# Kernel optimization log

Measured on AMD Instinct MI355X. Metric: run time of the kernel, lower is better.

## Reference

```python
import jax, jax.numpy as jnp
import numpy as np

NUM_HEADS = 4

def setup_inputs() -> dict:
    key = jax.random.key(0)
    ks = jax.random.split(key, 9)
    C = 256
    def w(k, shape, scale):
        return jax.random.normal(k, shape, dtype=jnp.float32) * scale
    s = 1.0 / np.sqrt(C)
    return {
        'x':  w(ks[0], (1, C, 48, 48), 1.0),
        'Wq': w(ks[1], (C, C), s), 'bq': w(ks[2], (C,), 0.01),
        'Wk': w(ks[3], (C, C), s), 'bk': w(ks[4], (C,), 0.01),
        'Wv': w(ks[5], (C, C), s), 'bv': w(ks[6], (C,), 0.01),
        'Wo': w(ks[7], (C, C), s), 'bo': w(ks[8], (C,), 0.01),
    }

def reference(x, Wq, bq, Wk, bk, Wv, bv, Wo, bo):
    # x: [B, C, H, W] (NCHW like torch). 1x1 convs == per-pixel matmuls in NHWC.
    B, C, H, W = x.shape
    nh = NUM_HEADS
    xt = jnp.transpose(x, (0, 2, 3, 1))                 # [B,H,W,C]
    q = xt @ Wq.T + bq                                  # [B,H,W,Ck]
    k = xt @ Wk.T + bk                                  # [B,H,W,Ck]
    v = xt @ Wv.T + bv                                  # [B,H,W,Cv]
    dk = q.shape[-1] // nh
    dv = v.shape[-1] // nh
    # split heads then FULLY flatten (batch*H*W*heads), as in the original
    qf = q.reshape(B * H * W * nh, dk) / jnp.sqrt(jnp.float32(dk))
    kf = k.reshape(B * H * W * nh, dk)
    vf = v.reshape(B * H * W * nh, dv)
    A = jax.nn.softmax(qf @ kf.T, axis=1)               # [N,N], N = B*H*W*nh
    # dropout is identity in eval mode
    O = A @ vf                                          # [N,dv]
    O = O.reshape(B, H, W, nh * dv)                     # heads folded back into channels
    out = O @ Wo.T + bo                                 # 1x1 output conv
    return jnp.transpose(out, (0, 3, 1, 2))             # [B,Cout,H,W]
```

## Files before the change

kernel.cpp:

```cpp
#include <hip/hip_runtime.h>
#include <stdint.h>

typedef __attribute__((ext_vector_type(4))) float f32x4;
typedef __attribute__((ext_vector_type(8))) short bf16x8;

#define MFMA(a, b, c) __builtin_amdgcn_mfma_f32_16x16x32_bf16(a, b, c, 0, 0, 0)

__device__ __forceinline__ short f2b(float f) {
    uint32_t u = __builtin_bit_cast(uint32_t, f);
    u += 0x7fffu + ((u >> 16) & 1u);
    return (short)(u >> 16);
}

__device__ __forceinline__ float ex2(float x) {
    float r; asm("v_exp_f32 %0, %1" : "=v"(r) : "v"(x)); return r;
}
__device__ __forceinline__ uint32_t cvtpk(float lo, float hi) {
    uint32_t r; asm("v_cvt_pk_bf16_f32 %0, %1, %2" : "=v"(r) : "v"(lo), "v"(hi)); return r;
}

typedef __attribute__((address_space(1))) const uint32_t gu32;
typedef __attribute__((address_space(3))) uint32_t su32;
__device__ __forceinline__ void stage16(const void* g, void* s) {
    __builtin_amdgcn_global_load_lds((gu32*)g, (su32*)s, 16, 0, 0);
}

__device__ __forceinline__ int FSW(int r) { return (r & 3) | (((r >> 3) & 1) << 2); }

#define QSCALE 0.1803368801111601f

__global__ __launch_bounds__(256) void k_prep(
    const float* __restrict__ x,
    const float* __restrict__ Wq, const float* __restrict__ Wk,
    const float* __restrict__ Wv, const float* __restrict__ Wo,
    short* __restrict__ Wall, short* __restrict__ xt) {
    __shared__ float tile[64][65];
    if (blockIdx.x < 1024) {
        int idx = blockIdx.x * 256 + threadIdx.x;
        int row = idx >> 8, col = idx & 255;
        float v;
        if (row < 256)      v = Wq[row * 256 + col];
        else if (row < 512) v = Wk[(row - 256) * 256 + col];
        else if (row < 768) v = Wv[(row - 512) * 256 + col];
        else                v = Wo[(row - 768) * 256 + col];
        Wall[idx] = f2b(v);
    } else {
        int b = blockIdx.x - 1024;
        int pbase = (b % 36) * 64, cbase = (b / 36) * 64;
        int tx = threadIdx.x & 63, tq = threadIdx.x >> 6;
        #pragma unroll
        for (int r = 0; r < 16; r++) {
            int row = tq * 16 + r;
            tile[row][tx] = x[(cbase + row) * 2304 + pbase + tx];
        }
        __syncthreads();
        #pragma unroll
        for (int r = 0; r < 16; r++) {
            int prow = tq * 16 + r;
            xt[(pbase + prow) * 256 + cbase + tx] = f2b(tile[tx][prow]);
        }
    }
}

__global__ __launch_bounds__(256) void k_gemm_qkv(
    const short* __restrict__ Wall, const short* __restrict__ xt,
    const float* __restrict__ bq, const float* __restrict__ bk, const float* __restrict__ bv,
    short* __restrict__ Qf, short* __restrict__ Kf, short* __restrict__ Vt) {
    int t = threadIdx.x, wave = t >> 6, lane = t & 63, lr = lane & 15, lg = lane >> 4;
    int obase = blockIdx.x * 64 + wave * 16;
    int pbase = blockIdx.y * 64;
    const short* arow  = Wall + (obase + lr) * 256 + lg * 8;
    const short* brow0 = xt + (pbase +  0 + lr) * 256 + lg * 8;
    const short* brow1 = xt + (pbase + 16 + lr) * 256 + lg * 8;
    const short* brow2 = xt + (pbase + 32 + lr) * 256 + lg * 8;
    const short* brow3 = xt + (pbase + 48 + lr) * 256 + lg * 8;
    f32x4 acc0 = {0,0,0,0}, acc1 = {0,0,0,0}, acc2 = {0,0,0,0}, acc3 = {0,0,0,0};
    #pragma unroll
    for (int ks = 0; ks < 8; ks++) {
        bf16x8 a = *(const bf16x8*)(arow + ks * 32);
        acc0 = MFMA(a, *(const bf16x8*)(brow0 + ks * 32), acc0);
        acc1 = MFMA(a, *(const bf16x8*)(brow1 + ks * 32), acc1);
        acc2 = MFMA(a, *(const bf16x8*)(brow2 + ks * 32), acc2);
        acc3 = MFMA(a, *(const bf16x8*)(brow3 + ks * 32), acc3);
    }
    int w_idx = obase >> 8;
    const float* bias = (w_idx == 0) ? bq : (w_idx == 1) ? bk : bv;
    f32x4 accs[4] = {acc0, acc1, acc2, acc3};
    #pragma unroll
    for (int i = 0; i < 4; i++) {
        int o = obase + 4 * lg + i;
        int oo = o & 255;
        float b = bias[oo];
        int h = oo >> 6, d = oo & 63;
        #pragma unroll
        for (int ct = 0; ct < 4; ct++) {
            int p = pbase + ct * 16 + lr;
            float val = accs[ct][i] + b;
            int n = p * 4 + h;
            if (w_idx == 0)      Qf[n * 64 + d] = f2b(val * QSCALE);
            else if (w_idx == 1) Kf[n * 64 + d] = f2b(val);
            else                 Vt[d * 9216 + n] = f2b(val);
        }
    }
}

__global__ __launch_bounds__(256) void k_attn(
    const short* __restrict__ Qf, const short* __restrict__ Kf,
    const short* __restrict__ Vt, int keysPer, int ntiles,
    float* __restrict__ pm, float* __restrict__ ps, float* __restrict__ pacc) {
    __shared__ short ktile[2][4096];
    __shared__ short vtile[2][4096];
    int t = threadIdx.x, wave = t >> 6, lane = t & 63, lr = lane & 15, lg = lane >> 4;
    int kb = blockIdx.y;
    int qbase = blockIdx.x * 64 + wave * 16;
    int kstart = kb * keysPer;

    const short* qrow = Qf + (qbase + lr) * 64 + lg * 8;
    bf16x8 q0 = *(const bf16x8*)(qrow);
    bf16x8 q1 = *(const bf16x8*)(qrow + 32);

    bf16x8 ones;
    #pragma unroll
    for (int i = 0; i < 8; i++) ones[i] = (short)0x3F80;

    int sr = lane >> 3, slot = lane & 7;
    int srow0 = wave * 16 + sr, srow1 = srow0 + 8;
    int col0 = (slot ^ FSW(srow0)) << 4;
    int col1 = (slot ^ FSW(srow1)) << 4;
    const char* kS0 = (const char*)Kf + (size_t)(kstart + srow0) * 128 + col0;
    const char* kS1 = (const char*)Kf + (size_t)(kstart + srow1) * 128 + col1;
    const char* vS0 = (const char*)Vt + (size_t)srow0 * 18432 + (size_t)kstart * 2 + col0;
    const char* vS1 = (const char*)Vt + (size_t)srow1 * 18432 + (size_t)kstart * 2 + col1;
    short* kD0[2] = { &ktile[0][wave * 1024], &ktile[1][wave * 1024] };
    short* kD1[2] = { kD0[0] + 512, kD0[1] + 512 };
    short* vD0[2] = { &vtile[0][wave * 1024], &vtile[1][wave * 1024] };
    short* vD1[2] = { vD0[0] + 512, vD0[1] + 512 };

    int perm = (lr & 3) + 8 * (lr >> 2);
    int cb = lg * 16;
    int kOffA0 = perm * 128       + (cb        ^ (FSW(perm) << 4));
    int kOffA1 = perm * 128       + ((cb + 64) ^ (FSW(perm) << 4));
    int kOffB0 = (perm + 4) * 128 + (cb        ^ (FSW(perm + 4) << 4));
    int kOffB1 = (perm + 4) * 128 + ((cb + 64) ^ (FSW(perm + 4) << 4));
    int vOff   = lr * 128         + (cb        ^ (FSW(lr) << 4));

    float mA = 0.f;
    f32x4 zv = {0,0,0,0};
    f32x4 cin = zv;
    f32x4 acc0 = zv, acc1 = zv, acc2 = zv, acc3 = zv, sacc = zv;

    stage16(kS0, kD0[0]); stage16(kS1, kD1[0]);
    stage16(vS0, vD0[0]); stage16(vS1, vD1[0]);

    for (int tt = 0; tt < ntiles; tt++) {
        __syncthreads();
        int buf = tt & 1;
        if (tt + 1 < ntiles) {
            size_t ko = (size_t)(tt + 1) * 8192, vo = (size_t)(tt + 1) * 128;
            stage16(kS0 + ko, kD0[buf ^ 1]); stage16(kS1 + ko, kD1[buf ^ 1]);
            stage16(vS0 + vo, vD0[buf ^ 1]); stage16(vS1 + vo, vD1[buf ^ 1]);
        }
        const char* kt = (const char*)&ktile[buf][0];
        const char* vt = (const char*)&vtile[buf][0];

        bf16x8 kA0 = *(const bf16x8*)(kt + kOffA0);
        bf16x8 kA1 = *(const bf16x8*)(kt + kOffA1);
        bf16x8 kB0 = *(const bf16x8*)(kt + kOffB0);
        bf16x8 kB1 = *(const bf16x8*)(kt + kOffB1);
        f32x4 st0 = MFMA(kA0, q0, cin); st0 = MFMA(kA1, q1, st0);
        f32x4 st1 = MFMA(kB0, q0, cin); st1 = MFMA(kB1, q1, st1);
        bf16x8 kC0 = *(const bf16x8*)(kt + 4096 + kOffA0);
        bf16x8 kC1 = *(const bf16x8*)(kt + 4096 + kOffA1);
        bf16x8 kE0 = *(const bf16x8*)(kt + 4096 + kOffB0);
        bf16x8 kE1 = *(const bf16x8*)(kt + 4096 + kOffB1);
        f32x4 st2 = MFMA(kC0, q0, cin); st2 = MFMA(kC1, q1, st2);
        f32x4 st3 = MFMA(kE0, q0, cin); st3 = MFMA(kE1, q1, st3);

        float tm = fmaxf(
            fmaxf(fmaxf(fmaxf(st0[0], st0[1]), fmaxf(st0[2], st0[3])),
                  fmaxf(fmaxf(st1[0], st1[1]), fmaxf(st1[2], st1[3]))),
            fmaxf(fmaxf(fmaxf(st2[0], st2[1]), fmaxf(st2[2], st2[3])),
                  fmaxf(fmaxf(st3[0], st3[1]), fmaxf(st3[2], st3[3]))));
        tm = fmaxf(fmaxf(tm, __shfl_xor(tm, 16)),
                   fmaxf(__shfl_xor(tm, 32), __shfl_xor(tm, 48)));
        if (!__all(tm <= 11.0f)) {
            float mn = fmaxf(tm, 0.f);
            float sc = ex2(-mn);
            acc0 *= sc; acc1 *= sc; acc2 *= sc; acc3 *= sc; sacc *= sc;
            mA += mn;
            f32x4 mnv = {mn, mn, mn, mn};
            cin -= mnv;
            st0 -= mnv; st1 -= mnv; st2 -= mnv; st3 -= mnv;
        }
        union { uint32_t w[4]; bf16x8 v; } pa, pb;
        pa.w[0] = cvtpk(ex2(st0[0]), ex2(st0[1]));
        pa.w[1] = cvtpk(ex2(st0[2]), ex2(st0[3]));
        pa.w[2] = cvtpk(ex2(st1[0]), ex2(st1[1]));
        pa.w[3] = cvtpk(ex2(st1[2]), ex2(st1[3]));
        pb.w[0] = cvtpk(ex2(st2[0]), ex2(st2[1]));
        pb.w[1] = cvtpk(ex2(st2[2]), ex2(st2[3]));
        pb.w[2] = cvtpk(ex2(st3[0]), ex2(st3[1]));
        pb.w[3] = cvtpk(ex2(st3[2]), ex2(st3[3]));

        bf16x8 v0a = *(const bf16x8*)(vt + vOff);
        bf16x8 v0b = *(const bf16x8*)(vt + (vOff ^ 64));
        bf16x8 v1a = *(const bf16x8*)(vt + vOff + 2048);
        bf16x8 v1b = *(const bf16x8*)(vt + ((vOff + 2048) ^ 64));
        bf16x8 v2a = *(const bf16x8*)(vt + vOff + 4096);
        bf16x8 v2b = *(const bf16x8*)(vt + ((vOff + 4096) ^ 64));
        bf16x8 v3a = *(const bf16x8*)(vt + vOff + 6144);
        bf16x8 v3b = *(const bf16x8*)(vt + ((vOff + 6144) ^ 64));
        acc0 = MFMA(v0a, pa.v, acc0); acc0 = MFMA(v0b, pb.v, acc0);
        acc1 = MFMA(v1a, pa.v, acc1); acc1 = MFMA(v1b, pb.v, acc1);
        acc2 = MFMA(v2a, pa.v, acc2); acc2 = MFMA(v2b, pb.v, acc2);
        acc3 = MFMA(v3a, pa.v, acc3); acc3 = MFMA(v3b, pb.v, acc3);
        sacc = MFMA(ones, pa.v, sacc); sacc = MFMA(ones, pb.v, sacc);
    }

    int g = blockIdx.x * 4 + wave;
    int pidx = kb * 576 + g;
    float* pa_ = pacc + (size_t)pidx * 1024 + lr * 64 + lg * 4;
    *(f32x4*)(pa_ +  0) = acc0;
    *(f32x4*)(pa_ + 16) = acc1;
    *(f32x4*)(pa_ + 32) = acc2;
    *(f32x4*)(pa_ + 48) = acc3;
    if (lg == 0) {
        pm[pidx * 16 + lr] = mA;
        ps[pidx * 16 + lr] = sacc[0];
    }
}

__global__ __launch_bounds__(256) void k_attn_combine(
    const float* __restrict__ pm, const float* __restrict__ ps,
    const float* __restrict__ pacc, short* __restrict__ Of, int nsplit) {
    int qb = blockIdx.x, t = threadIdx.x;
    int q = t >> 4, dv4 = (t & 15) * 4;
    float mg = -1e30f;
    for (int s = 0; s < nsplit; s++)
        mg = fmaxf(mg, pm[(s * 576 + qb) * 16 + q]);
    float S = 0.f;
    f32x4 O = {0, 0, 0, 0};
    for (int s = 0; s < nsplit; s++) {
        float e = ex2(pm[(s * 576 + qb) * 16 + q] - mg);
        S += ps[(s * 576 + qb) * 16 + q] * e;
        f32x4 pv = *(const f32x4*)(pacc + (size_t)(s * 576 + qb) * 1024 + q * 64 + dv4);
        O += pv * e;
    }
    float inv = 1.0f / S;
    uint32_t w0 = cvtpk(O[0] * inv, O[1] * inv);
    uint32_t w1 = cvtpk(O[2] * inv, O[3] * inv);
    int n = qb * 16 + q, p = n >> 2, hh = n & 3;
    uint2 pk; pk.x = w0; pk.y = w1;
    *(uint2*)(&Of[p * 256 + hh * 64 + dv4]) = pk;
}

__global__ __launch_bounds__(256) void k_gemm_out(
    const short* __restrict__ Wo_bf, const short* __restrict__ Of,
    const float* __restrict__ bo, float* __restrict__ out) {
    int t = threadIdx.x, wave = t >> 6, lane = t & 63, lr = lane & 15, lg = lane >> 4;
    int obase = blockIdx.x * 64 + wave * 16;
    int pbase = blockIdx.y * 64;
    const short* arow  = Wo_bf + (obase + lr) * 256 + lg * 8;
    const short* brow0 = Of + (pbase +  0 + lr) * 256 + lg * 8;
    const short* brow1 = Of + (pbase + 16 + lr) * 256 + lg * 8;
    const short* brow2 = Of + (pbase + 32 + lr) * 256 + lg * 8;
    const short* brow3 = Of + (pbase + 48 + lr) * 256 + lg * 8;
    f32x4 acc0 = {0,0,0,0}, acc1 = {0,0,0,0}, acc2 = {0,0,0,0}, acc3 = {0,0,0,0};
    #pragma unroll
    for (int ks = 0; ks < 8; ks++) {
        bf16x8 a = *(const bf16x8*)(arow + ks * 32);
        acc0 = MFMA(a, *(const bf16x8*)(brow0 + ks * 32), acc0);
        acc1 = MFMA(a, *(const bf16x8*)(brow1 + ks * 32), acc1);
        acc2 = MFMA(a, *(const bf16x8*)(brow2 + ks * 32), acc2);
        acc3 = MFMA(a, *(const bf16x8*)(brow3 + ks * 32), acc3);
    }
    f32x4 accs[4] = {acc0, acc1, acc2, acc3};
    #pragma unroll
    for (int i = 0; i < 4; i++) {
        int o = obase + 4 * lg + i;
        float b = bo[o];
        #pragma unroll
        for (int ct = 0; ct < 4; ct++) {
            int p = pbase + ct * 16 + lr;
            out[o * 2304 + p] = accs[ct][i] + b;
        }
    }
}

extern "C" void kernel_launch(void* const* d_in, const int* in_sizes, int n_in,
                              void* d_out, int out_size, void* d_ws, size_t ws_size,
                              hipStream_t stream) {
    const float* x  = (const float*)d_in[0];
    const float* Wq = (const float*)d_in[1];
    const float* bq = (const float*)d_in[2];
    const float* Wk = (const float*)d_in[3];
    const float* bk = (const float*)d_in[4];
    const float* Wv = (const float*)d_in[5];
    const float* bv = (const float*)d_in[6];
    const float* Wo = (const float*)d_in[7];
    const float* bo = (const float*)d_in[8];

    char* ws = (char*)d_ws;
    short* Wall = (short*)(ws);
    short* xt   = (short*)(ws + 524288);
    short* Qf   = (short*)(ws + 1703936);
    short* Kf   = (short*)(ws + 2883584);
    short* Vt   = (short*)(ws + 4063232);
    short* Of   = (short*)(ws + 5242880);
    float* pm   = (float*)(ws + 6422528);
    float* ps   = (float*)(ws + 6717440);
    float* pacc = (float*)(ws + 7012352);
    float* out  = (float*)d_out;

    int nsplit = (ws_size >= (size_t)7012352 + 8u * 2359296u) ? 8 : 4;
    int keysPer = 9216 / nsplit;
    int ntiles = keysPer / 64;

    k_prep<<<1168, 256, 0, stream>>>(x, Wq, Wk, Wv, Wo, Wall, xt);
    k_gemm_qkv<<<dim3(12, 36), 256, 0, stream>>>(Wall, xt, bq, bk, bv, Qf, Kf, Vt);
    k_attn<<<dim3(144, nsplit), 256, 0, stream>>>(Qf, Kf, Vt, keysPer, ntiles, pm, ps, pacc);
    k_attn_combine<<<576, 256, 0, stream>>>(pm, ps, pacc, Of, nsplit);
    k_gemm_out<<<dim3(4, 36), 256, 0, stream>>>(Wall + 768 * 256, Of, bo, out);
}
```

Before: 80.35 us.

## Process two query tiles per wave, store bf16 partials, double split count

Each wave now handles two 16-query tiles against each staged K/V tile, so every LDS load of K and V feeds twice as many MFMAs and per-key staging cost is halved. The grid is halved in x and the key split is raised to 16 (or 8) to keep enough blocks. Partial accumulators are written as bf16 instead of fp32 to shrink combine traffic. The costs are higher register pressure and possibly lower occupancy, plus extra rounding in the partial sums.

```diff
diff --git a/kernel.cpp b/kernel.cpp
--- a/kernel.cpp
+++ b/kernel.cpp
@@ -17,6 +17,12 @@
 }
 __device__ __forceinline__ uint32_t cvtpk(float lo, float hi) {
     uint32_t r; asm("v_cvt_pk_bf16_f32 %0, %1, %2" : "=v"(r) : "v"(lo), "v"(hi)); return r;
+}
+__device__ __forceinline__ float lo2f(uint32_t u) {
+    return __builtin_bit_cast(float, (uint32_t)(u << 16));
+}
+__device__ __forceinline__ float hi2f(uint32_t u) {
+    return __builtin_bit_cast(float, (uint32_t)(u & 0xffff0000u));
 }
 
 typedef __attribute__((address_space(1))) const uint32_t gu32;
@@ -107,17 +113,20 @@
 __global__ __launch_bounds__(256) void k_attn(
     const short* __restrict__ Qf, const short* __restrict__ Kf,
     const short* __restrict__ Vt, int keysPer, int ntiles,
-    float* __restrict__ pm, float* __restrict__ ps, float* __restrict__ pacc) {
+    float* __restrict__ pm, float* __restrict__ ps, uint32_t* __restrict__ pacc) {
     __shared__ short ktile[2][4096];
     __shared__ short vtile[2][4096];
     int t = threadIdx.x, wave = t >> 6, lane = t & 63, lr = lane & 15, lg = lane >> 4;
     int kb = blockIdx.y;
-    int qbase = blockIdx.x * 64 + wave * 16;
+    int qbase = blockIdx.x * 128 + wave * 16;
     int kstart = kb * keysPer;
 
-    const short* qrow = Qf + (qbase + lr) * 64 + lg * 8;
-    bf16x8 q0 = *(const bf16x8*)(qrow);
-    bf16x8 q1 = *(const bf16x8*)(qrow + 32);
+    const short* qrowA = Qf + (qbase + lr) * 64 + lg * 8;
+    bf16x8 qA0 = *(const bf16x8*)(qrowA);
+    bf16x8 qA1 = *(const bf16x8*)(qrowA + 32);
+    const short* qrowB = qrowA + 64 * 64;
+    bf16x8 qB0 = *(const bf16x8*)(qrowB);
+    bf16x8 qB1 = *(const bf16x8*)(qrowB + 32);
 
     bf16x8 ones;
     #pragma unroll
@@ -144,10 +153,11 @@
     int kOffB1 = (perm + 4) * 128 + ((cb + 64) ^ (FSW(perm + 4) << 4));
     int vOff   = lr * 128         + (cb        ^ (FSW(lr) << 4));
 
-    float mA = 0.f;
+    float mA = 0.f, mB = 0.f;
     f32x4 zv = {0,0,0,0};
-    f32x4 cin = zv;
-    f32x4 acc0 = zv, acc1 = zv, acc2 = zv, acc3 = zv, sacc = zv;
+    f32x4 cinA = zv, cinB = zv;
+    f32x4 accA0 = zv, accA1 = zv, accA2 = zv, accA3 = zv, saccA = zv;
+    f32x4 accB0 = zv, accB1 = zv, accB2 = zv, accB3 = zv, saccB = zv;
 
     stage16(kS0, kD0[0]); stage16(kS1, kD1[0]);
     stage16(vS0, vD0[0]); stage16(vS1, vD1[0]);
@@ -167,40 +177,61 @@
         bf16x8 kA1 = *(const bf16x8*)(kt + kOffA1);
         bf16x8 kB0 = *(const bf16x8*)(kt + kOffB0);
         bf16x8 kB1 = *(const bf16x8*)(kt + kOffB1);
-        f32x4 st0 = MFMA(kA0, q0, cin); st0 = MFMA(kA1, q1, st0);
-        f32x4 st1 = MFMA(kB0, q0, cin); st1 = MFMA(kB1, q1, st1);
-        bf16x8 kC0 = *(const bf16x8*)(kt + 4096 + kOffA0);
-        bf16x8 kC1 = *(const bf16x8*)(kt + 4096 + kOffA1);
-        bf16x8 kE0 = *(const bf16x8*)(kt + 4096 + kOffB0);
-        bf16x8 kE1 = *(const bf16x8*)(kt + 4096 + kOffB1);
-        f32x4 st2 = MFMA(kC0, q0, cin); st2 = MFMA(kC1, q1, st2);
-        f32x4 st3 = MFMA(kE0, q0, cin); st3 = MFMA(kE1, q1, st3);
-
-        float tm = fmaxf(
-            fmaxf(fmaxf(fmaxf(st0[0], st0[1]), fmaxf(st0[2], st0[3])),
-                  fmaxf(fmaxf(st1[0], st1[1]), fmaxf(st1[2], st1[3]))),
-            fmaxf(fmaxf(fmaxf(st2[0], st2[1]), fmaxf(st2[2], st2[3])),
-                  fmaxf(fmaxf(st3[0], st3[1]), fmaxf(st3[2], st3[3]))));
-        tm = fmaxf(fmaxf(tm, __shfl_xor(tm, 16)),
-                   fmaxf(__shfl_xor(tm, 32), __shfl_xor(tm, 48)));
-        if (!__all(tm <= 11.0f)) {
-            float mn = fmaxf(tm, 0.f);
-            float sc = ex2(-mn);
-            acc0 *= sc; acc1 *= sc; acc2 *= sc; acc3 *= sc; sacc *= sc;
-            mA += mn;
-            f32x4 mnv = {mn, mn, mn, mn};
-            cin -= mnv;
-            st0 -= mnv; st1 -= mnv; st2 -= mnv; st3 -= mnv;
-        }
-        union { uint32_t w[4]; bf16x8 v; } pa, pb;
-        pa.w[0] = cvtpk(ex2(st0[0]), ex2(st0[1]));
-        pa.w[1] = cvtpk(ex2(st0[2]), ex2(st0[3]));
-        pa.w[2] = cvtpk(ex2(st1[0]), ex2(st1[1]));
-        pa.w[3] = cvtpk(ex2(st1[2]), ex2(st1[3]));
-        pb.w[0] = cvtpk(ex2(st2[0]), ex2(st2[1]));
-        pb.w[1] = cvtpk(ex2(st2[2]), ex2(st2[3]));
-        pb.w[2] = cvtpk(ex2(st3[0]), ex2(st3[1]));
-        pb.w[3] = cvtpk(ex2(st3[2]), ex2(st3[3]));
+        f32x4 sA0 = MFMA(kA0, qA0, cinA); sA0 = MFMA(kA1, qA1, sA0);
+        f32x4 sA1 = MFMA(kB0, qA0, cinA); sA1 = MFMA(kB1, qA1, sA1);
+        f32x4 sB0 = MFMA(kA0, qB0, cinB); sB0 = MFMA(kA1, qB1, sB0);
+        f32x4 sB1 = MFMA(kB0, qB0, cinB); sB1 = MFMA(kB1, qB1, sB1);
+        kA0 = *(const bf16x8*)(kt + 4096 + kOffA0);
+        kA1 = *(const bf16x8*)(kt + 4096 + kOffA1);
+        kB0 = *(const bf16x8*)(kt + 4096 + kOffB0);
+        kB1 = *(const bf16x8*)(kt + 4096 + kOffB1);
+        f32x4 sA2 = MFMA(kA0, qA0, cinA); sA2 = MFMA(kA1, qA1, sA2);
+        f32x4 sA3 = MFMA(kB0, qA0, cinA); sA3 = MFMA(kB1, qA1, sA3);
+        f32x4 sB2 = MFMA(kA0, qB0, cinB); sB2 = MFMA(kA1, qB1, sB2);
+        f32x4 sB3 = MFMA(kB0, qB0, cinB); sB3 = MFMA(kB1, qB1, sB3);
+
+        float tmA = fmaxf(
+            fmaxf(fmaxf(fmaxf(sA0[0], sA0[1]), fmaxf(sA0[2], sA0[3])),
+                  fmaxf(fmaxf(sA1[0], sA1[1]), fmaxf(sA1[2], sA1[3]))),
+            fmaxf(fmaxf(fmaxf(sA2[0], sA2[1]), fmaxf(sA2[2], sA2[3])),
+                  fmaxf(fmaxf(sA3[0], sA3[1]), fmaxf(sA3[2], sA3[3]))));
+        float tmB = fmaxf(
+            fmaxf(fmaxf(fmaxf(sB0[0], sB0[1]), fmaxf(sB0[2], sB0[3])),
+                  fmaxf(fmaxf(sB1[0], sB1[1]), fmaxf(sB1[2], sB1[3]))),
+            fmaxf(fmaxf(fmaxf(sB2[0], sB2[1]), fmaxf(sB2[2], sB2[3])),
+                  fmaxf(fmaxf(sB3[0], sB3[1]), fmaxf(sB3[2], sB3[3]))));
+        tmA = fmaxf(fmaxf(tmA, __shfl_xor(tmA, 16)),
+                    fmaxf(__shfl_xor(tmA, 32), __shfl_xor(tmA, 48)));
+        tmB = fmaxf(fmaxf(tmB, __shfl_xor(tmB, 16)),
+                    fmaxf(__shfl_xor(tmB, 32), __shfl_xor(tmB, 48)));
+        if (!__all((tmA <= 11.0f) && (tmB <= 11.0f))) {
+            float mnA = fmaxf(tmA, 0.f), mnB = fmaxf(tmB, 0.f);
+            float scA = ex2(-mnA), scB = ex2(-mnB);
+            accA0 *= scA; accA1 *= scA; accA2 *= scA; accA3 *= scA; saccA *= scA;
+            accB0 *= scB; accB1 *= scB; accB2 *= scB; accB3 *= scB; saccB *= scB;
+            mA += mnA; mB += mnB;
+            f32x4 mvA = {mnA, mnA, mnA, mnA}, mvB = {mnB, mnB, mnB, mnB};
+            cinA -= mvA; cinB -= mvB;
+            sA0 -= mvA; sA1 -= mvA; sA2 -= mvA; sA3 -= mvA;
+            sB0 -= mvB; sB1 -= mvB; sB2 -= mvB; sB3 -= mvB;
+        }
+        union { uint32_t w[4]; bf16x8 v; } paA, pbA, paB, pbB;
+        paA.w[0] = cvtpk(ex2(sA0[0]), ex2(sA0[1]));
+        paA.w[1] = cvtpk(ex2(sA0[2]), ex2(sA0[3]));
+        paA.w[2] = cvtpk(ex2(sA1[0]), ex2(sA1[1]));
+        paA.w[3] = cvtpk(ex2(sA1[2]), ex2(sA1[3]));
+        pbA.w[0] = cvtpk(ex2(sA2[0]), ex2(sA2[1]));
+        pbA.w[1] = cvtpk(ex2(sA2[2]), ex2(sA2[3]));
+        pbA.w[2] = cvtpk(ex2(sA3[0]), ex2(sA3[1]));
+        pbA.w[3] = cvtpk(ex2(sA3[2]), ex2(sA3[3]));
+        paB.w[0] = cvtpk(ex2(sB0[0]), ex2(sB0[1]));
+        paB.w[1] = cvtpk(ex2(sB0[2]), ex2(sB0[3]));
+        paB.w[2] = cvtpk(ex2(sB1[0]), ex2(sB1[1]));
+        paB.w[3] = cvtpk(ex2(sB1[2]), ex2(sB1[3]));
+        pbB.w[0] = cvtpk(ex2(sB2[0]), ex2(sB2[1]));
+        pbB.w[1] = cvtpk(ex2(sB2[2]), ex2(sB2[3]));
+        pbB.w[2] = cvtpk(ex2(sB3[0]), ex2(sB3[1]));
+        pbB.w[3] = cvtpk(ex2(sB3[2]), ex2(sB3[3]));
 
         bf16x8 v0a = *(const bf16x8*)(vt + vOff);
         bf16x8 v0b = *(const bf16x8*)(vt + (vOff ^ 64));
@@ -210,29 +241,41 @@
         bf16x8 v2b = *(const bf16x8*)(vt + ((vOff + 4096) ^ 64));
         bf16x8 v3a = *(const bf16x8*)(vt + vOff + 6144);
         bf16x8 v3b = *(const bf16x8*)(vt + ((vOff + 6144) ^ 64));
-        acc0 = MFMA(v0a, pa.v, acc0); acc0 = MFMA(v0b, pb.v, acc0);
-        acc1 = MFMA(v1a, pa.v, acc1); acc1 = MFMA(v1b, pb.v, acc1);
-        acc2 = MFMA(v2a, pa.v, acc2); acc2 = MFMA(v2b, pb.v, acc2);
-        acc3 = MFMA(v3a, pa.v, acc3); acc3 = MFMA(v3b, pb.v, acc3);
-        sacc = MFMA(ones, pa.v, sacc); sacc = MFMA(ones, pb.v, sacc);
-    }
-
-    int g = blockIdx.x * 4 + wave;
-    int pidx = kb * 576 + g;
-    float* pa_ = pacc + (size_t)pidx * 1024 + lr * 64 + lg * 4;
-    *(f32x4*)(pa_ +  0) = acc0;
-    *(f32x4*)(pa_ + 16) = acc1;
-    *(f32x4*)(pa_ + 32) = acc2;
-    *(f32x4*)(pa_ + 48) = acc3;
+        accA0 = MFMA(v0a, paA.v, accA0); accA0 = MFMA(v0b, pbA.v, accA0);
+        accA1 = MFMA(v1a, paA.v, accA1); accA1 = MFMA(v1b, pbA.v, accA1);
+        accA2 = MFMA(v2a, paA.v, accA2); accA2 = MFMA(v2b, pbA.v, accA2);
+        accA3 = MFMA(v3a, paA.v, accA3); accA3 = MFMA(v3b, pbA.v, accA3);
+        saccA = MFMA(ones, paA.v, saccA); saccA = MFMA(ones, pbA.v, saccA);
+        accB0 = MFMA(v0a, paB.v, accB0); accB0 = MFMA(v0b, pbB.v, accB0);
+        accB1 = MFMA(v1a, paB.v, accB1); accB1 = MFMA(v1b, pbB.v, accB1);
+        accB2 = MFMA(v2a, paB.v, accB2); accB2 = MFMA(v2b, pbB.v, accB2);
+        accB3 = MFMA(v3a, paB.v, accB3); accB3 = MFMA(v3b, pbB.v, accB3);
+        saccB = MFMA(ones, paB.v, saccB); saccB = MFMA(ones, pbB.v, saccB);
+    }
+
+    int gA = blockIdx.x * 8 + wave;
+    int gB = gA + 4;
+    int pidxA = kb * 576 + gA, pidxB = kb * 576 + gB;
+    uint2* outA = (uint2*)pacc + (size_t)pidxA * 256 + lr * 16 + lg;
+    uint2* outB = (uint2*)pacc + (size_t)pidxB * 256 + lr * 16 + lg;
+    uint2 w;
+    w.x = cvtpk(accA0[0], accA0[1]); w.y = cvtpk(accA0[2], accA0[3]); outA[0]  = w;
+    w.x = cvtpk(accA1[0], accA1[1]); w.y = cvtpk(accA1[2], accA1[3]); outA[4]  = w;
+    w.x = cvtpk(accA2[0], accA2[1]); w.y = cvtpk(accA2[2], accA2[3]); outA[8]  = w;
+    w.x = cvtpk(accA3[0], accA3[1]); w.y = cvtpk(accA3[2], accA3[3]); outA[12] = w;
+    w.x = cvtpk(accB0[0], accB0[1]); w.y = cvtpk(accB0[2], accB0[3]); outB[0]  = w;
+    w.x = cvtpk(accB1[0], accB1[1]); w.y = cvtpk(accB1[2], accB1[3]); outB[4]  = w;
+    w.x = cvtpk(accB2[0], accB2[1]); w.y = cvtpk(accB2[2], accB2[3]); outB[8]  = w;
+    w.x = cvtpk(accB3[0], accB3[1]); w.y = cvtpk(accB3[2], accB3[3]); outB[12] = w;
     if (lg == 0) {
-        pm[pidx * 16 + lr] = mA;
-        ps[pidx * 16 + lr] = sacc[0];
+        pm[pidxA * 16 + lr] = mA;  ps[pidxA * 16 + lr] = saccA[0];
+        pm[pidxB * 16 + lr] = mB;  ps[pidxB * 16 + lr] = saccB[0];
     }
 }
 
 __global__ __launch_bounds__(256) void k_attn_combine(
     const float* __restrict__ pm, const float* __restrict__ ps,
-    const float* __restrict__ pacc, short* __restrict__ Of, int nsplit) {
+    const uint32_t* __restrict__ pacc, short* __restrict__ Of, int nsplit) {
     int qb = blockIdx.x, t = threadIdx.x;
     int q = t >> 4, dv4 = (t & 15) * 4;
     float mg = -1e30f;
@@ -243,8 +286,9 @@
     for (int s = 0; s < nsplit; s++) {
         float e = ex2(pm[(s * 576 + qb) * 16 + q] - mg);
         S += ps[(s * 576 + qb) * 16 + q] * e;
-        f32x4 pv = *(const f32x4*)(pacc + (size_t)(s * 576 + qb) * 1024 + q * 64 + dv4);
-        O += pv * e;
+        uint2 v = ((const uint2*)pacc)[(size_t)(s * 576 + qb) * 256 + t];
+        O[0] += lo2f(v.x) * e; O[1] += hi2f(v.x) * e;
+        O[2] += lo2f(v.y) * e; O[3] += hi2f(v.y) * e;
     }
     float inv = 1.0f / S;
     uint32_t w0 = cvtpk(O[0] * inv, O[1] * inv);
@@ -308,17 +352,17 @@
     short* Vt   = (short*)(ws + 4063232);
     short* Of   = (short*)(ws + 5242880);
     float* pm   = (float*)(ws + 6422528);
-    float* ps   = (float*)(ws + 6717440);
-    float* pacc = (float*)(ws + 7012352);
+    float* ps   = (float*)(ws + 7012352);
+    uint32_t* pacc = (uint32_t*)(ws + 7602176);
     float* out  = (float*)d_out;
 
-    int nsplit = (ws_size >= (size_t)7012352 + 8u * 2359296u) ? 8 : 4;
+    int nsplit = (ws_size >= (size_t)7602176 + 16u * 576u * 2048u) ? 16 : 8;
     int keysPer = 9216 / nsplit;
     int ntiles = keysPer / 64;
 
     k_prep<<<1168, 256, 0, stream>>>(x, Wq, Wk, Wv, Wo, Wall, xt);
     k_gemm_qkv<<<dim3(12, 36), 256, 0, stream>>>(Wall, xt, bq, bk, bv, Qf, Kf, Vt);
-    k_attn<<<dim3(144, nsplit), 256, 0, stream>>>(Qf, Kf, Vt, keysPer, ntiles, pm, ps, pacc);
+    k_attn<<<dim3(72, nsplit), 256, 0, stream>>>(Qf, Kf, Vt, keysPer, ntiles, pm, ps, pacc);
     k_attn_combine<<<576, 256, 0, stream>>>(pm, ps, pacc, Of, nsplit);
     k_gemm_out<<<dim3(4, 36), 256, 0, stream>>>(Wall + 768 * 256, Of, bo, out);
 }
```

New measurement: 82.93 us. 3.2% more time.
